# Performance work log

Hardware: AMD Instinct MI355X
Metric: run time of the kernel (lower is better)

## Reference

```python
import jax, jax.numpy as jnp
import numpy as np
from jax import lax

TAU_MEM = 10.0
V_THRESHOLD = 1.0
V_RESET = 0.0
V_REST = 0.0
SURROGATE_BETA = 1.0
DT = 1.0

BATCH, N_STEPS, N_NEURONS = 32, 1000, 1024


@jax.custom_vjp
def spike_fn(v):
    # Heaviside step at threshold; surrogate sigmoid gradient in bwd.
    return (v >= V_THRESHOLD).astype(v.dtype)

def _spike_fwd(v):
    return spike_fn(v), v

def _spike_bwd(v, g):
    sig = jax.nn.sigmoid(SURROGATE_BETA * (v - V_THRESHOLD))
    return (g * SURROGATE_BETA * sig * (1.0 - sig),)

spike_fn.defvjp(_spike_fwd, _spike_bwd)


def setup_inputs() -> dict:
    key = jax.random.key(0)
    k1, _ = jax.random.split(key)
    input_current = jax.random.normal(k1, (BATCH, N_STEPS, N_NEURONS), dtype=jnp.float32)
    v_init = jnp.zeros((BATCH, N_NEURONS), dtype=jnp.float32)
    return {"input_current": input_current, "v_init": v_init}


def reference(input_current, v_init):
    # input_current: [B, T, N]; v_init: [B, N]
    def step(v, i_t):
        # Euler update of leaky membrane: tau dV/dt = -(V - V_rest) + I
        v = v + ((-(v - V_REST) + i_t) / TAU_MEM) * DT
        s = spike_fn(v)
        v = v * (1.0 - s) + V_RESET * s  # reset on spike
        return v, (s, v)

    i_tbn = jnp.transpose(input_current, (1, 0, 2))  # [T, B, N]
    _, (spikes, voltages) = lax.scan(step, v_init, i_tbn)
    spikes = jnp.transpose(spikes, (1, 0, 2))    # [B, T, N]
    voltages = jnp.transpose(voltages, (1, 0, 2))
    return spikes, voltages
```

## Files before the change

### kernel.cpp

```cpp
#include <hip/hip_runtime.h>


constexpr int B = 32;
constexpr int T = 1000;
constexpr int N = 1024;
constexpr int U = 20;
constexpr int NBLK = T / U;

__device__ __forceinline__ void lif_steps(const float (&buf)[U], float& v,
                                          float* __restrict__ sp,
                                          float* __restrict__ vp, int t0)
{
    float sb[U], vb[U];
    #pragma unroll
    for (int j = 0; j < U; ++j) {
        float nv = v + (buf[j] - v) / 10.0f;
        const bool fire = (nv >= 1.0f);
        sb[j] = fire ? 1.0f : 0.0f;
        nv = fire ? 0.0f : nv;
        vb[j] = nv;
        v = nv;
    }
    #pragma unroll
    for (int j = 0; j < U; ++j) {
        sp[(size_t)(t0 + j) * N] = sb[j];
        vp[(size_t)(t0 + j) * N] = vb[j];
    }
}

__global__ __launch_bounds__(64) void lif_kernel(
    const float* __restrict__ in,
    const float* __restrict__ v0,
    float* __restrict__ spk,
    float* __restrict__ vol)
{
    const int idx = blockIdx.x * 64 + threadIdx.x;
    const int b = idx >> 10;
    const int n = idx & (N - 1);
    const size_t base = (size_t)b * T * N + n;

    const float* ip = in  + base;
    float*       sp = spk + base;
    float*       vp = vol + base;

    float v = v0[idx];

    float bufA[U], bufB[U];
    #pragma unroll
    for (int j = 0; j < U; ++j) bufA[j] = ip[(size_t)j * N];

    for (int blk = 0; blk < NBLK; blk += 2) {
        const int tA = blk * U;
        const int tB = tA + U;
        const int tC = tA + 2 * U;

        #pragma unroll
        for (int j = 0; j < U; ++j) bufB[j] = ip[(size_t)(tB + j) * N];

        lif_steps(bufA, v, sp, vp, tA);

        if (tC < T) {
            #pragma unroll
            for (int j = 0; j < U; ++j) bufA[j] = ip[(size_t)(tC + j) * N];
        }

        lif_steps(bufB, v, sp, vp, tB);
    }
}

extern "C" void kernel_launch(void* const* d_in, const int* in_sizes, int n_in,
                              void* d_out, int out_size, void* d_ws, size_t ws_size,
                              hipStream_t stream) {
    const float* in = (const float*)d_in[0];
    const float* v0 = (const float*)d_in[1];
    float* spk = (float*)d_out;
    float* vol = (float*)d_out + (size_t)B * T * N;

    const int threads = 64;
    const int blocks  = (B * N) / threads;
    lif_kernel<<<blocks, threads, 0, stream>>>(in, v0, spk, vol);
}
```

Baseline: 362.0 us.

## Split LIF scan into boundary pass plus parallel time-chunk pass

Adds a first kernel that runs the full recurrence but stores only the membrane voltage at each of 10 chunk boundaries into workspace, with no spike or voltage outputs. A second kernel then launches 10x more threads, each recomputing one 100-step chunk from its boundary value and writing the outputs. The goal is more parallelism than 32K threads provide, so the heavy output writes can saturate bandwidth. The cost is reading the input twice and running two launches, and there is a fallback to the fused kernel when the workspace is too small.

```diff
diff --git a/kernel.cpp b/kernel.cpp
--- a/kernel.cpp
+++ b/kernel.cpp
@@ -1,19 +1,67 @@
 #include <hip/hip_runtime.h>
 
 
-constexpr int B = 32;
-constexpr int T = 1000;
-constexpr int N = 1024;
-constexpr int U = 20;
-constexpr int NBLK = T / U;
+constexpr int B  = 32;
+constexpr int T  = 1000;
+constexpr int N  = 1024;
+constexpr int BN = B * N;
+constexpr int C  = 10;
+constexpr int TC = T / C;
 
-__device__ __forceinline__ void lif_steps(const float (&buf)[U], float& v,
-                                          float* __restrict__ sp,
-                                          float* __restrict__ vp, int t0)
+constexpr int U1  = 20;
+constexpr int NB1 = T / U1;
+
+__global__ __launch_bounds__(64) void lif_boundary(
+    const float* __restrict__ in,
+    const float* __restrict__ v0,
+    float* __restrict__ bnd)
 {
-    float sb[U], vb[U];
+    const int idx = blockIdx.x * 64 + threadIdx.x;
+    const int b = idx >> 10;
+    const int n = idx & (N - 1);
+    const float* ip = in + (size_t)b * T * N + n;
+
+    float v = v0[idx];
+    float bufA[U1], bufB[U1];
     #pragma unroll
-    for (int j = 0; j < U; ++j) {
+    for (int j = 0; j < U1; ++j) bufA[j] = ip[(size_t)j * N];
+
+    for (int blk = 0; blk < NB1; blk += 2) {
+        const int tA = blk * U1, tB = tA + U1, tN = tA + 2 * U1;
+
+        #pragma unroll
+        for (int j = 0; j < U1; ++j) bufB[j] = ip[(size_t)(tB + j) * N];
+        #pragma unroll
+        for (int j = 0; j < U1; ++j) {
+            float nv = v + (bufA[j] - v) / 10.0f;
+            v = (nv >= 1.0f) ? 0.0f : nv;
+        }
+        if ((tA + U1) % TC == 0 && (tA + U1) < T)
+            bnd[(size_t)((tA + U1) / TC - 1) * BN + idx] = v;
+
+        if (tN < T) {
+            #pragma unroll
+            for (int j = 0; j < U1; ++j) bufA[j] = ip[(size_t)(tN + j) * N];
+        }
+        #pragma unroll
+        for (int j = 0; j < U1; ++j) {
+            float nv = v + (bufB[j] - v) / 10.0f;
+            v = (nv >= 1.0f) ? 0.0f : nv;
+        }
+        if ((tB + U1) % TC == 0 && (tB + U1) < T)
+            bnd[(size_t)((tB + U1) / TC - 1) * BN + idx] = v;
+    }
+}
+
+constexpr int U2 = 20;
+
+__device__ __forceinline__ void chunk_steps(const float (&buf)[U2], float& v,
+                                            float* __restrict__ sp,
+                                            float* __restrict__ vp, int t0)
+{
+    float sb[U2], vb[U2];
+    #pragma unroll
+    for (int j = 0; j < U2; ++j) {
         float nv = v + (buf[j] - v) / 10.0f;
         const bool fire = (nv >= 1.0f);
         sb[j] = fire ? 1.0f : 0.0f;
@@ -22,49 +70,97 @@
         v = nv;
     }
     #pragma unroll
-    for (int j = 0; j < U; ++j) {
+    for (int j = 0; j < U2; ++j) {
         sp[(size_t)(t0 + j) * N] = sb[j];
         vp[(size_t)(t0 + j) * N] = vb[j];
     }
 }
 
-__global__ __launch_bounds__(64) void lif_kernel(
+__global__ __launch_bounds__(256) void lif_chunks(
     const float* __restrict__ in,
     const float* __restrict__ v0,
+    const float* __restrict__ bnd,
     float* __restrict__ spk,
     float* __restrict__ vol)
+{
+    const int g   = blockIdx.x * 256 + threadIdx.x;
+    const int idx = g & (BN - 1);
+    const int c   = g >> 15;
+    const int b   = idx >> 10;
+    const int n   = idx & (N - 1);
+    const size_t base = (size_t)b * T * N + (size_t)c * TC * N + n;
+    const float* ip = in  + base;
+    float*       sp = spk + base;
+    float*       vp = vol + base;
+
+    float v = (c == 0) ? v0[idx] : bnd[(size_t)(c - 1) * BN + idx];
+
+    float bufA[U2], bufB[U2];
+    #pragma unroll
+    for (int j = 0; j < U2; ++j) bufA[j] = ip[(size_t)j * N];
+    #pragma unroll
+    for (int j = 0; j < U2; ++j) bufB[j] = ip[(size_t)(U2 + j) * N];
+    chunk_steps(bufA, v, sp, vp, 0);
+    #pragma unroll
+    for (int j = 0; j < U2; ++j) bufA[j] = ip[(size_t)(2 * U2 + j) * N];
+    chunk_steps(bufB, v, sp, vp, U2);
+    #pragma unroll
+    for (int j = 0; j < U2; ++j) bufB[j] = ip[(size_t)(3 * U2 + j) * N];
+    chunk_steps(bufA, v, sp, vp, 2 * U2);
+    #pragma unroll
+    for (int j = 0; j < U2; ++j) bufA[j] = ip[(size_t)(4 * U2 + j) * N];
+    chunk_steps(bufB, v, sp, vp, 3 * U2);
+    chunk_steps(bufA, v, sp, vp, 4 * U2);
+}
+
+__device__ __forceinline__ void fb_steps(const float (&buf)[U1], float& v,
+                                         float* __restrict__ sp,
+                                         float* __restrict__ vp, int t0)
+{
+    float sb[U1], vb[U1];
+    #pragma unroll
+    for (int j = 0; j < U1; ++j) {
+        float nv = v + (buf[j] - v) / 10.0f;
+        const bool fire = (nv >= 1.0f);
+        sb[j] = fire ? 1.0f : 0.0f;
+        nv = fire ? 0.0f : nv;
+        vb[j] = nv;
+        v = nv;
+    }
+    #pragma unroll
+    for (int j = 0; j < U1; ++j) {
+        sp[(size_t)(t0 + j) * N] = sb[j];
+        vp[(size_t)(t0 + j) * N] = vb[j];
+    }
+}
+
+__global__ __launch_bounds__(64) void lif_fused(
+    const float* __restrict__ in, const float* __restrict__ v0,
+    float* __restrict__ spk, float* __restrict__ vol)
 {
     const int idx = blockIdx.x * 64 + threadIdx.x;
     const int b = idx >> 10;
     const int n = idx & (N - 1);
     const size_t base = (size_t)b * T * N + n;
-
-    const float* ip = in  + base;
-    float*       sp = spk + base;
-    float*       vp = vol + base;
+    const float* ip = in + base;
+    float* sp = spk + base;
+    float* vp = vol + base;
 
     float v = v0[idx];
+    float bufA[U1], bufB[U1];
+    #pragma unroll
+    for (int j = 0; j < U1; ++j) bufA[j] = ip[(size_t)j * N];
 
-    float bufA[U], bufB[U];
-    #pragma unroll
-    for (int j = 0; j < U; ++j) bufA[j] = ip[(size_t)j * N];
-
-    for (int blk = 0; blk < NBLK; blk += 2) {
-        const int tA = blk * U;
-        const int tB = tA + U;
-        const int tC = tA + 2 * U;
-
+    for (int blk = 0; blk < NB1; blk += 2) {
+        const int tA = blk * U1, tB = tA + U1, tN = tA + 2 * U1;
         #pragma unroll
-        for (int j = 0; j < U; ++j) bufB[j] = ip[(size_t)(tB + j) * N];
-
-        lif_steps(bufA, v, sp, vp, tA);
-
-        if (tC < T) {
+        for (int j = 0; j < U1; ++j) bufB[j] = ip[(size_t)(tB + j) * N];
+        fb_steps(bufA, v, sp, vp, tA);
+        if (tN < T) {
             #pragma unroll
-            for (int j = 0; j < U; ++j) bufA[j] = ip[(size_t)(tC + j) * N];
+            for (int j = 0; j < U1; ++j) bufA[j] = ip[(size_t)(tN + j) * N];
         }
-
-        lif_steps(bufB, v, sp, vp, tB);
+        fb_steps(bufB, v, sp, vp, tB);
     }
 }
 
@@ -76,7 +172,12 @@
     float* spk = (float*)d_out;
     float* vol = (float*)d_out + (size_t)B * T * N;
 
-    const int threads = 64;
-    const int blocks  = (B * N) / threads;
-    lif_kernel<<<blocks, threads, 0, stream>>>(in, v0, spk, vol);
+    const size_t bnd_bytes = (size_t)(C - 1) * BN * sizeof(float);
+    if (ws_size >= bnd_bytes) {
+        float* bnd = (float*)d_ws;
+        lif_boundary<<<BN / 64, 64, 0, stream>>>(in, v0, bnd);
+        lif_chunks<<<(C * BN) / 256, 256, 0, stream>>>(in, v0, bnd, spk, vol);
+    } else {
+        lif_fused<<<BN / 64, 64, 0, stream>>>(in, v0, spk, vol);
+    }
 }
```

After: 405.5 us. 1.12x slower.
